# Kernel optimization log

Hardware: AMD Instinct MI355X
Metric: run time of the kernel (lower is better)

Reference implementation:

```python
import jax, jax.numpy as jnp
import numpy as np

ALPHA = 0.5
MOM = 0.9            # momentum m in the recurrence
ACTIVATION = "tanh"
NUM_LAYERS = 2
CACHE = 32           # GROUP size
NK = 4               # n_kernel_feats
B, N, E = 4, 4096, 128


def _act(T):
    if ACTIVATION == "leaky-relu":
        return jax.nn.leaky_relu(T)
    elif ACTIVATION == "tanh":
        return jnp.tanh(T)
    return T


def _group_indices(N, cache, stage):
    # vectorized group_pos_to_index_v2 over all (group_nr, pos_in_group)
    m = N // cache
    o = np.arange(cache)
    s = 0 if stage == 0 else (1 << (stage - 1)) % m
    g = np.arange(m)[:, None]
    block = (g + o[None, :] * s) % m
    return jnp.asarray(block * cache + o[None, :])  # [m, cache], a permutation of 0..N-1


def _ncn_layer(X, Xa, W, stage):
    B, N, E = X.shape
    ce = E // NK
    m = N // CACHE
    idx = _group_indices(N, CACHE, stage)           # [m, cache]
    Wi = W[:E].reshape(NK, ce)
    Wj = W[E:].reshape(NK, ce)
    # gather groups: [B, m, NK, cache, ce]
    xg = jnp.moveaxis(X.reshape(B, N, NK, ce)[:, idx], 3, 2)
    xag = jnp.moveaxis(Xa.reshape(B, N, NK, ce)[:, idx], 3, 2)

    def step(carry, j):
        xi, xa = carry                               # [B, m, NK, cache, ce]
        xj = jnp.take(xi, j, axis=3)                 # [B, m, NK, ce]  (row start_j)
        sim = (jnp.einsum('bgnke,ne->bgnk', xi, Wi)
               + jnp.einsum('bgne,ne->bgn', xj, Wj)[..., None])   # [B, m, NK, cache]
        T = ALPHA * xi + (1.0 - ALPHA) * sim[..., None] * xj[:, :, :, None, :]
        F = _act(T)
        ya = MOM * xa + (1.0 - MOM) * F
        yi = MOM * xi + (1.0 - MOM) * ya
        return (yi, ya), None

    (yi, ya), _ = jax.lax.scan(step, (xg, xag), jnp.arange(CACHE))

    # scatter back; idx is a permutation so .set reproduces the += into zeros
    def scatter(v):
        v = jnp.moveaxis(v, 2, 3).reshape(B, m * CACHE, E)
        return jnp.zeros((B, N, E), v.dtype).at[:, idx.reshape(-1)].set(v)

    return scatter(yi), scatter(ya)


def setup_inputs() -> dict:
    key = jax.random.key(0)
    k1, k2, k3 = jax.random.split(key, 3)
    x = jax.random.normal(k1, (B, N, E), jnp.float32)
    xa = jax.random.normal(k2, (B, N, E), jnp.float32)
    W = jax.random.normal(k3, (NUM_LAYERS, 2 * E), jnp.float32)
    return {"x": x, "xa": xa, "W": W}


def reference(x, xa, W):
    for l in range(NUM_LAYERS):
        x, xa = _ncn_layer(x, xa, W[l], l)
    return x, xa
```

## Files before the change

### kernel.cpp

```cpp
#include <hip/hip_runtime.h>


namespace {
constexpr int kB = 4;
constexpr int kN = 4096;
constexpr int kE = 128;
constexpr int kCE = 32;
constexpr int kH  = 16;
constexpr int kCache = 32;
constexpr int kM = kN / kCache;

typedef __attribute__((ext_vector_type(2))) float f32x2;

__device__ __forceinline__ f32x2 pk_fma(f32x2 a, f32x2 b, f32x2 c) {
    return __builtin_elementwise_fma(a, b, c);
}
__device__ __forceinline__ float bperm_f(int addr, float v) {
    return __int_as_float(__builtin_amdgcn_ds_bpermute(addr, __float_as_int(v)));
}
}

#define LD16(dst, ptr)                                                  \
    {                                                                   \
        const float4* p4 = reinterpret_cast<const float4*>(ptr);        \
        float4 q0 = p4[0], q1 = p4[1], q2 = p4[2], q3 = p4[3];          \
        dst##0 = f32x2{q0.x, q0.y}; dst##1 = f32x2{q0.z, q0.w};         \
        dst##2 = f32x2{q1.x, q1.y}; dst##3 = f32x2{q1.z, q1.w};         \
        dst##4 = f32x2{q2.x, q2.y}; dst##5 = f32x2{q2.z, q2.w};         \
        dst##6 = f32x2{q3.x, q3.y}; dst##7 = f32x2{q3.z, q3.w};         \
    }

#define ST16(src, ptr)                                                  \
    {                                                                   \
        float4* p4 = reinterpret_cast<float4*>(ptr);                    \
        p4[0] = float4{src##0 .x, src##0 .y, src##1 .x, src##1 .y};     \
        p4[1] = float4{src##2 .x, src##2 .y, src##3 .x, src##3 .y};     \
        p4[2] = float4{src##4 .x, src##4 .y, src##5 .x, src##5 .y};     \
        p4[3] = float4{src##6 .x, src##6 .y, src##7 .x, src##7 .y};     \
    }

#define PULL(q)                                                         \
    f32x2 xj##q;                                                        \
    xj##q .x = bperm_f(srcaddr, xi##q .x);                              \
    xj##q .y = bperm_f(srcaddr, xi##q .y);

#define UPD(q)                                                          \
    {                                                                   \
        f32x2 arg = pk_fma(xj##q, sv, xi##q * l12);                     \
        f32x2 t2;                                                       \
        t2.x = __builtin_amdgcn_exp2f(arg.x);                           \
        t2.y = __builtin_amdgcn_exp2f(arg.y);                           \
        f32x2 den = t2 + one;                                           \
        f32x2 rc;                                                       \
        rc.x = __builtin_amdgcn_rcpf(den.x);                            \
        rc.y = __builtin_amdgcn_rcpf(den.y);                            \
        xa##q = pk_fma(m02, rc, pk_fma(c9, xa##q, c01));                \
        xi##q = pk_fma(c01, xa##q, xi##q * c9);                         \
    }

__global__ void __launch_bounds__(64)
__attribute__((amdgpu_waves_per_eu(2, 2)))
ncn_layer_kernel(
    const float* __restrict__ x_in, const float* __restrict__ xa_in,
    const float* __restrict__ Wl,
    float* __restrict__ x_out, float* __restrict__ xa_out,
    int s)
{
    const int blk = blockIdx.x;
    const int n   = blk & 3;
    const int g   = (blk >> 2) & (kM - 1);
    const int b   = blk >> 9;
    const int t   = threadIdx.x;
    const int o   = t & 31;
    const int h   = t >> 5;

    const int r = (((g + o * s) & (kM - 1)) << 5) + o;
    const size_t base = ((size_t)(b * kN + r)) * kE + n * kCE + h * kH;

    constexpr float L1 = 1.4426950408889634f;

    f32x2 xi0, xi1, xi2, xi3, xi4, xi5, xi6, xi7;
    f32x2 xa0, xa1, xa2, xa3, xa4, xa5, xa6, xa7;
    f32x2 wi0, wi1, wi2, wi3, wi4, wi5, wi6, wi7;
    f32x2 wj0, wj1, wj2, wj3, wj4, wj5, wj6, wj7;

    LD16(xi, x_in + base);
    LD16(xa, xa_in + base);
    LD16(wi, Wl + n * kCE + h * kH);
    LD16(wj, Wl + kE + n * kCE + h * kH);

    {
        const f32x2 l12 = {L1, L1};
        wi0 *= l12; wi1 *= l12; wi2 *= l12; wi3 *= l12;
        wi4 *= l12; wi5 *= l12; wi6 *= l12; wi7 *= l12;
        wj0 *= l12; wj1 *= l12; wj2 *= l12; wj3 *= l12;
        wj4 *= l12; wj5 *= l12; wj6 *= l12; wj7 *= l12;
    }

    const int srcbase = (t & 32) * 4;

#pragma unroll 2
    for (int j = 0; j < kCache; ++j) {
        const int srcaddr = srcbase + j * 4;

        PULL(0) PULL(1) PULL(2) PULL(3) PULL(4) PULL(5) PULL(6) PULL(7)

        f32x2 A = xi0 * wi0;
        f32x2 B = xi1 * wi1;
        f32x2 C = xj0 * wj0;
        f32x2 D = xj1 * wj1;
        A = pk_fma(xi2, wi2, A); B = pk_fma(xi3, wi3, B);
        C = pk_fma(xj2, wj2, C); D = pk_fma(xj3, wj3, D);
        A = pk_fma(xi4, wi4, A); B = pk_fma(xi5, wi5, B);
        C = pk_fma(xj4, wj4, C); D = pk_fma(xj5, wj5, D);
        A = pk_fma(xi6, wi6, A); B = pk_fma(xi7, wi7, B);
        C = pk_fma(xj6, wj6, C); D = pk_fma(xj7, wj7, D);
        f32x2 uv = (A + B) + (C + D);
        float u  = uv.x + uv.y;

        const float sim = u + __shfl_xor(u, 32, 64);
        const f32x2 sv  = {sim, sim};
        const f32x2 l12 = {L1, L1};
        const f32x2 one = {1.0f, 1.0f};
        const f32x2 m02 = {-0.2f, -0.2f};
        const f32x2 c9  = {0.9f, 0.9f};
        const f32x2 c01 = {0.1f, 0.1f};

        UPD(0) UPD(1) UPD(2) UPD(3) UPD(4) UPD(5) UPD(6) UPD(7)
    }

    ST16(xi, x_out + base);
    ST16(xa, xa_out + base);
}

extern "C" void kernel_launch(void* const* d_in, const int* in_sizes, int n_in,
                              void* d_out, int out_size, void* d_ws, size_t ws_size,
                              hipStream_t stream) {
    const float* x  = (const float*)d_in[0];
    const float* xa = (const float*)d_in[1];
    const float* W  = (const float*)d_in[2];

    const size_t plane = (size_t)kB * kN * kE;

    float* x_mid  = (float*)d_ws;
    float* xa_mid = x_mid + plane;

    float* x_out  = (float*)d_out;
    float* xa_out = x_out + plane;

    const dim3 grid(kB * kM * 4);
    const dim3 block(64);

    ncn_layer_kernel<<<grid, block, 0, stream>>>(x, xa, W, x_mid, xa_mid, 0);
    ncn_layer_kernel<<<grid, block, 0, stream>>>(x_mid, xa_mid, W + 2 * kE,
                                                 x_out, xa_out, 1);
}
```

Measured before the change: 121.9 us.

## Fuse both layers into one persistent kernel with a grid-wide barrier

The two per-layer launches become one kernel of 256 blocks with 8 waves each, separated by an atomic-counter grid barrier in workspace memory that is cleared by a memset before launch. It also pre-scales x by log2(e) and W by ln2 so the inner loop skips one multiply per element. The aim is to remove the second launch and its gap; in exchange it adds a memset, the barrier spin, and a deadlock risk if the 256 blocks cannot all be resident at once.

```diff
diff --git a/kernel.cpp b/kernel.cpp
--- a/kernel.cpp
+++ b/kernel.cpp
@@ -9,6 +9,8 @@
 constexpr int kH  = 16;
 constexpr int kCache = 32;
 constexpr int kM = kN / kCache;
+constexpr int kBlocks = 256;
+constexpr int kThreads = 512;
 
 typedef __attribute__((ext_vector_type(2))) float f32x2;
 
@@ -20,33 +22,41 @@
 }
 }
 
-#define LD16(dst, ptr)                                                  \
+#define LD16S(dst, ptr, sc)                                             \
     {                                                                   \
         const float4* p4 = reinterpret_cast<const float4*>(ptr);        \
         float4 q0 = p4[0], q1 = p4[1], q2 = p4[2], q3 = p4[3];          \
-        dst##0 = f32x2{q0.x, q0.y}; dst##1 = f32x2{q0.z, q0.w};         \
-        dst##2 = f32x2{q1.x, q1.y}; dst##3 = f32x2{q1.z, q1.w};         \
-        dst##4 = f32x2{q2.x, q2.y}; dst##5 = f32x2{q2.z, q2.w};         \
-        dst##6 = f32x2{q3.x, q3.y}; dst##7 = f32x2{q3.z, q3.w};         \
+        dst##0 = f32x2{q0.x * sc, q0.y * sc};                           \
+        dst##1 = f32x2{q0.z * sc, q0.w * sc};                           \
+        dst##2 = f32x2{q1.x * sc, q1.y * sc};                           \
+        dst##3 = f32x2{q1.z * sc, q1.w * sc};                           \
+        dst##4 = f32x2{q2.x * sc, q2.y * sc};                           \
+        dst##5 = f32x2{q2.z * sc, q2.w * sc};                           \
+        dst##6 = f32x2{q3.x * sc, q3.y * sc};                           \
+        dst##7 = f32x2{q3.z * sc, q3.w * sc};                           \
     }
 
-#define ST16(src, ptr)                                                  \
+#define ST16S(src, ptr, sc)                                             \
     {                                                                   \
         float4* p4 = reinterpret_cast<float4*>(ptr);                    \
-        p4[0] = float4{src##0 .x, src##0 .y, src##1 .x, src##1 .y};     \
-        p4[1] = float4{src##2 .x, src##2 .y, src##3 .x, src##3 .y};     \
-        p4[2] = float4{src##4 .x, src##4 .y, src##5 .x, src##5 .y};     \
-        p4[3] = float4{src##6 .x, src##6 .y, src##7 .x, src##7 .y};     \
+        p4[0] = float4{src##0 .x * sc, src##0 .y * sc,                  \
+                       src##1 .x * sc, src##1 .y * sc};                 \
+        p4[1] = float4{src##2 .x * sc, src##2 .y * sc,                  \
+                       src##3 .x * sc, src##3 .y * sc};                 \
+        p4[2] = float4{src##4 .x * sc, src##4 .y * sc,                  \
+                       src##5 .x * sc, src##5 .y * sc};                 \
+        p4[3] = float4{src##6 .x * sc, src##6 .y * sc,                  \
+                       src##7 .x * sc, src##7 .y * sc};                 \
     }
 
 #define PULL(q)                                                         \
-    f32x2 xj##q;                                                        \
-    xj##q .x = bperm_f(srcaddr, xi##q .x);                              \
-    xj##q .y = bperm_f(srcaddr, xi##q .y);
+    f32x2 zj##q;                                                        \
+    zj##q .x = bperm_f(srcaddr, zi##q .x);                              \
+    zj##q .y = bperm_f(srcaddr, zi##q .y);
 
 #define UPD(q)                                                          \
     {                                                                   \
-        f32x2 arg = pk_fma(xj##q, sv, xi##q * l12);                     \
+        f32x2 arg = pk_fma(zj##q, sv, zi##q);                           \
         f32x2 t2;                                                       \
         t2.x = __builtin_amdgcn_exp2f(arg.x);                           \
         t2.y = __builtin_amdgcn_exp2f(arg.y);                           \
@@ -55,82 +65,106 @@
         rc.x = __builtin_amdgcn_rcpf(den.x);                            \
         rc.y = __builtin_amdgcn_rcpf(den.y);                            \
         xa##q = pk_fma(m02, rc, pk_fma(c9, xa##q, c01));                \
-        xi##q = pk_fma(c01, xa##q, xi##q * c9);                         \
+        zi##q = pk_fma(cL1, xa##q, zi##q * c9);                         \
     }
 
-__global__ void __launch_bounds__(64)
-__attribute__((amdgpu_waves_per_eu(2, 2)))
-ncn_layer_kernel(
+#define SCAN_LAYER()                                                    \
+    _Pragma("unroll 2")                                                 \
+    for (int j = 0; j < kCache; ++j) {                                  \
+        const int srcaddr = srcbase + j * 4;                            \
+        PULL(0) PULL(1) PULL(2) PULL(3) PULL(4) PULL(5) PULL(6) PULL(7) \
+        f32x2 A = zi0 * wi0;                                            \
+        f32x2 Bv = zi1 * wi1;                                           \
+        f32x2 C = zj0 * wj0;                                            \
+        f32x2 D = zj1 * wj1;                                            \
+        A  = pk_fma(zi2, wi2, A);  Bv = pk_fma(zi3, wi3, Bv);           \
+        C  = pk_fma(zj2, wj2, C);  D  = pk_fma(zj3, wj3, D);            \
+        A  = pk_fma(zi4, wi4, A);  Bv = pk_fma(zi5, wi5, Bv);           \
+        C  = pk_fma(zj4, wj4, C);  D  = pk_fma(zj5, wj5, D);            \
+        A  = pk_fma(zi6, wi6, A);  Bv = pk_fma(zi7, wi7, Bv);           \
+        C  = pk_fma(zj6, wj6, C);  D  = pk_fma(zj7, wj7, D);            \
+        f32x2 uv = (A + Bv) + (C + D);                                  \
+        float u  = uv.x + uv.y;                                         \
+        const float sim = u + __shfl_xor(u, 32, 64);                    \
+        const f32x2 sv = {sim, sim};                                    \
+        UPD(0) UPD(1) UPD(2) UPD(3) UPD(4) UPD(5) UPD(6) UPD(7)         \
+    }
+
+__global__ void __launch_bounds__(kThreads, 2) ncn_fused_kernel(
     const float* __restrict__ x_in, const float* __restrict__ xa_in,
-    const float* __restrict__ Wl,
+    const float* __restrict__ W,
+    float* __restrict__ x_mid, float* __restrict__ xa_mid,
     float* __restrict__ x_out, float* __restrict__ xa_out,
-    int s)
+    unsigned* __restrict__ bar_cnt, unsigned* __restrict__ bar_gen)
 {
-    const int blk = blockIdx.x;
-    const int n   = blk & 3;
-    const int g   = (blk >> 2) & (kM - 1);
-    const int b   = blk >> 9;
-    const int t   = threadIdx.x;
-    const int o   = t & 31;
-    const int h   = t >> 5;
+    const int tid  = threadIdx.x;
+    const int wave = tid >> 6;
+    const int lane = tid & 63;
+    const int id   = blockIdx.x * 8 + wave;
+    const int n    = id & 3;
+    const int g    = (id >> 2) & (kM - 1);
+    const int b    = id >> 9;
+    const int o    = lane & 31;
+    const int h    = lane >> 5;
 
-    const int r = (((g + o * s) & (kM - 1)) << 5) + o;
-    const size_t base = ((size_t)(b * kN + r)) * kE + n * kCE + h * kH;
+    constexpr float L1   = 1.4426950408889634f;
+    constexpr float iL1  = 0.6931471805599453f;
+    const f32x2 one = {1.0f, 1.0f};
+    const f32x2 m02 = {-0.2f, -0.2f};
+    const f32x2 c9  = {0.9f, 0.9f};
+    const f32x2 c01 = {0.1f, 0.1f};
+    const f32x2 cL1 = {0.1f * L1, 0.1f * L1};
 
-    constexpr float L1 = 1.4426950408889634f;
+    const int srcbase = (lane & 32) * 4;
 
-    f32x2 xi0, xi1, xi2, xi3, xi4, xi5, xi6, xi7;
+    f32x2 zi0, zi1, zi2, zi3, zi4, zi5, zi6, zi7;
     f32x2 xa0, xa1, xa2, xa3, xa4, xa5, xa6, xa7;
     f32x2 wi0, wi1, wi2, wi3, wi4, wi5, wi6, wi7;
     f32x2 wj0, wj1, wj2, wj3, wj4, wj5, wj6, wj7;
 
-    LD16(xi, x_in + base);
-    LD16(xa, xa_in + base);
-    LD16(wi, Wl + n * kCE + h * kH);
-    LD16(wj, Wl + kE + n * kCE + h * kH);
+    const int r0 = (g << 5) + o;
+    const size_t base0 = ((size_t)(b * kN + r0)) * kE + n * kCE + h * kH;
 
-    {
-        const f32x2 l12 = {L1, L1};
-        wi0 *= l12; wi1 *= l12; wi2 *= l12; wi3 *= l12;
-        wi4 *= l12; wi5 *= l12; wi6 *= l12; wi7 *= l12;
-        wj0 *= l12; wj1 *= l12; wj2 *= l12; wj3 *= l12;
-        wj4 *= l12; wj5 *= l12; wj6 *= l12; wj7 *= l12;
+    LD16S(zi, x_in + base0, L1);
+    LD16S(xa, xa_in + base0, 1.0f);
+    LD16S(wi, W + n * kCE + h * kH, iL1);
+    LD16S(wj, W + kE + n * kCE + h * kH, iL1);
+
+    SCAN_LAYER();
+
+    ST16S(zi, x_mid + base0, iL1);
+    ST16S(xa, xa_mid + base0, 1.0f);
+
+    __threadfence();
+    __syncthreads();
+    if (tid == 0) {
+        unsigned arrived = __hip_atomic_fetch_add(
+            bar_cnt, 1u, __ATOMIC_ACQ_REL, __HIP_MEMORY_SCOPE_AGENT) + 1;
+        if (arrived == (unsigned)kBlocks) {
+            __hip_atomic_store(bar_gen, 1u, __ATOMIC_RELEASE,
+                               __HIP_MEMORY_SCOPE_AGENT);
+        } else {
+            while (__hip_atomic_load(bar_gen, __ATOMIC_ACQUIRE,
+                                     __HIP_MEMORY_SCOPE_AGENT) == 0u) {
+                __builtin_amdgcn_s_sleep(2);
+            }
+        }
     }
+    __syncthreads();
+    __threadfence();
 
-    const int srcbase = (t & 32) * 4;
+    const int r1 = (((g + o) & (kM - 1)) << 5) + o;
+    const size_t base1 = ((size_t)(b * kN + r1)) * kE + n * kCE + h * kH;
 
-#pragma unroll 2
-    for (int j = 0; j < kCache; ++j) {
-        const int srcaddr = srcbase + j * 4;
+    LD16S(zi, x_mid + base1, L1);
+    LD16S(xa, xa_mid + base1, 1.0f);
+    LD16S(wi, W + 2 * kE + n * kCE + h * kH, iL1);
+    LD16S(wj, W + 3 * kE + n * kCE + h * kH, iL1);
 
-        PULL(0) PULL(1) PULL(2) PULL(3) PULL(4) PULL(5) PULL(6) PULL(7)
+    SCAN_LAYER();
 
-        f32x2 A = xi0 * wi0;
-        f32x2 B = xi1 * wi1;
-        f32x2 C = xj0 * wj0;
-        f32x2 D = xj1 * wj1;
-        A = pk_fma(xi2, wi2, A); B = pk_fma(xi3, wi3, B);
-        C = pk_fma(xj2, wj2, C); D = pk_fma(xj3, wj3, D);
-        A = pk_fma(xi4, wi4, A); B = pk_fma(xi5, wi5, B);
-        C = pk_fma(xj4, wj4, C); D = pk_fma(xj5, wj5, D);
-        A = pk_fma(xi6, wi6, A); B = pk_fma(xi7, wi7, B);
-        C = pk_fma(xj6, wj6, C); D = pk_fma(xj7, wj7, D);
-        f32x2 uv = (A + B) + (C + D);
-        float u  = uv.x + uv.y;
-
-        const float sim = u + __shfl_xor(u, 32, 64);
-        const f32x2 sv  = {sim, sim};
-        const f32x2 l12 = {L1, L1};
-        const f32x2 one = {1.0f, 1.0f};
-        const f32x2 m02 = {-0.2f, -0.2f};
-        const f32x2 c9  = {0.9f, 0.9f};
-        const f32x2 c01 = {0.1f, 0.1f};
-
-        UPD(0) UPD(1) UPD(2) UPD(3) UPD(4) UPD(5) UPD(6) UPD(7)
-    }
-
-    ST16(xi, x_out + base);
-    ST16(xa, xa_out + base);
+    ST16S(zi, x_out + base1, iL1);
+    ST16S(xa, xa_out + base1, 1.0f);
 }
 
 extern "C" void kernel_launch(void* const* d_in, const int* in_sizes, int n_in,
@@ -142,16 +176,16 @@
 
     const size_t plane = (size_t)kB * kN * kE;
 
-    float* x_mid  = (float*)d_ws;
+    unsigned* bar_cnt = (unsigned*)d_ws;
+    unsigned* bar_gen = (unsigned*)((char*)d_ws + 256);
+    float* x_mid  = (float*)((char*)d_ws + 1024);
     float* xa_mid = x_mid + plane;
 
     float* x_out  = (float*)d_out;
     float* xa_out = x_out + plane;
 
-    const dim3 grid(kB * kM * 4);
-    const dim3 block(64);
+    hipMemsetAsync(d_ws, 0, 512, stream);
 
-    ncn_layer_kernel<<<grid, block, 0, stream>>>(x, xa, W, x_mid, xa_mid, 0);
-    ncn_layer_kernel<<<grid, block, 0, stream>>>(x_mid, xa_mid, W + 2 * kE,
-                                                 x_out, xa_out, 1);
+    ncn_fused_kernel<<<dim3(kBlocks), dim3(kThreads), 0, stream>>>(
+        x, xa, W, x_mid, xa_mid, x_out, xa_out, bar_cnt, bar_gen);
 }
```

New measurement: 242.5 us. 1.99x slower.
